# Kernel optimization log

Hardware: AMD Instinct MI355X
Metric: run time of the kernel (lower is better)

Reference implementation:

```python
import jax, jax.numpy as jnp
import numpy as np

ALPHA, BETA, GAMMA = 1.0, 1.0, 0.7
WIN = 11
C1 = 0.01 ** 2
C2 = 0.03 ** 2


def get_sobel_kernels(n1=1, n2=2, n3=2):
    a = np.asarray
    Sx = a([[[-n1, 0, n1], [-n2, 0, n2], [-n1, 0, n1]],
            [[-n2, 0, n2], [-n3 * n2, 0, n3 * n2], [-n2, 0, n2]],
            [[-n1, 0, n1], [-n2, 0, n2], [-n1, 0, n1]]])
    Sy = a([[[-n1, -n2, -n1], [0, 0, 0], [n1, n2, n1]],
            [[-n2, -n3 * n2, -n2], [0, 0, 0], [n2, n3 * n2, n2]],
            [[-n1, -n2, -n1], [0, 0, 0], [n1, n2, n1]]])
    Sz = a([[[-n1, -n2, -n1], [-n2, -n3 * n2, -n2], [-n1, -n2, -n1]],
            [[0, 0, 0], [0, 0, 0], [0, 0, 0]],
            [[n1, n2, n1], [n2, n3 * n2, n2], [n1, n2, n1]]])
    Sd11 = a([[[0, n1, n2], [-n1, 0, n1], [-n2, -n1, 0]],
              [[0, n2, n2 * n3], [-n2, 0, n2], [-n2 * n3, -n2, 0]],
              [[0, n1, n2], [-n1, 0, n1], [-n2, -n1, 0]]])
    Sd12 = a([[[-n2, -n1, 0], [-n1, 0, n1], [0, n1, n2]],
              [[-n2 * n3, -n2, 0], [-n2, 0, n2], [0, n2, n2 * n3]],
              [[-n2, -n1, 0], [-n1, 0, n1], [0, n1, n2]]])
    Sd21 = Sd11.T
    Sd22 = Sd12.T
    Sd31 = a([-S.T for S in Sd11.T])
    Sd32 = a([S.T for S in Sd12.T])
    return np.stack([Sx, Sy, Sz, Sd11, Sd12, Sd21, Sd22, Sd31, Sd32]).astype(np.float32)

# (9,1,3,3,3) fused sobel bank -- single grouped conv instead of 9 launches
SOBEL_W = jnp.asarray(get_sobel_kernels()[:, None])


def _gauss1d():
    g = jnp.exp(-(jnp.arange(WIN, dtype=jnp.float32) - WIN // 2) ** 2 / (2 * 1.5 ** 2))
    return g / g.sum()

G1D = _gauss1d()


def conv3d(x, w):
    return jax.lax.conv_general_dilated(
        x, w, window_strides=(1, 1, 1), padding='SAME',
        dimension_numbers=('NCDHW', 'OIDHW', 'NCDHW'))


def gauss_filter(x):
    # separable 11-tap gaussian along D, H, W (== full 11^3 window, zero-padded SAME)
    x = conv3d(x, G1D.reshape(1, 1, WIN, 1, 1))
    x = conv3d(x, G1D.reshape(1, 1, 1, WIN, 1))
    x = conv3d(x, G1D.reshape(1, 1, 1, 1, WIN))
    return x


def edge_map(img):
    # GradEdge3D.__call__ with a=1, C=1
    B, C, D, H, W = img.shape
    xp = jnp.pad(img, ((0, 0), (0, 0), (1, 1), (1, 1), (1, 1)), mode='reflect')
    g = conv3d(xp, SOBEL_W)                       # (B, 9, D+2, H+2, W+2)
    gm = jnp.sqrt(jnp.sum((g + 1e-6) ** 2 + 1e-6, axis=1))  # (B, D+2, H+2, W+2)
    gm = gm[:, 1:-1, 1:-1, 1:-1]
    norm = (gm - gm.min()) / (gm.max() - gm.min() + 1e-6)
    return norm.reshape(B, 1, D, H, W)


def ssim_value(pred, target):
    mu_p = gauss_filter(pred)
    mu_t = gauss_filter(target)
    mu_p2, mu_t2, mu_pt = mu_p ** 2, mu_t ** 2, mu_p * mu_t
    sig_p = gauss_filter(pred * pred) - mu_p2
    sig_t = gauss_filter(target * target) - mu_t2
    sig_pt = gauss_filter(pred * target) - mu_pt
    ssim_map = ((2 * mu_pt + C1) * (2 * sig_pt + C2)) / ((mu_p2 + mu_t2 + C1) * (sig_p + sig_t + C2))
    return 1.0 - ssim_map.mean()


def setup_inputs() -> dict:
    key = jax.random.key(0)
    k1, k2 = jax.random.split(key)
    shape = (2, 1, 128, 128, 128)
    return {
        'pred': jax.random.uniform(k1, shape, dtype=jnp.float32),
        'target': jax.random.uniform(k2, shape, dtype=jnp.float32),
    }


def reference(pred, target):
    loss_mse = jnp.mean((pred - target) ** 2)
    loss_ssim = ssim_value(pred, target)
    # GMELoss3D: lam_errors=[(1.0, L1Loss())], reduction='sum'
    loss_gme = 1e-6 + jnp.mean(jnp.abs(edge_map(pred) - edge_map(target)))
    total = ALPHA * loss_mse + BETA * loss_ssim + GAMMA * loss_gme
    return (total, loss_mse, loss_ssim, loss_gme)
```

## Files before the change

kernel.cpp:

```cpp
#include <hip/hip_runtime.h>


#define VOL 4194304
#define HV  2097152

typedef _Float16 h2 __attribute__((ext_vector_type(2)));
typedef _Float16 h4 __attribute__((ext_vector_type(4)));
typedef _Float16 h8 __attribute__((ext_vector_type(8)));

constexpr float GW[11] = {
    0.00102838f, 0.00759876f, 0.03600077f, 0.10936070f, 0.21300554f,
    0.26601173f,
    0.21300554f, 0.10936070f, 0.03600077f, 0.00759876f, 0.00102838f};



__device__ __forceinline__ void wblur_body(
    const float* __restrict__ p, const float* __restrict__ t,
    _Float16* __restrict__ A, double* __restrict__ mseB, const int bidx,
    char* __restrict__ pool, float* __restrict__ redw) {
  float (* __restrict__ sr)[138] = (float (*)[138])pool;
  float (* __restrict__ dr)[138] = (float (*)[138])(pool + 8832);
  const int tid = threadIdx.x;
  const int gbase = bidx << 11;
  if (tid < 160) {
    const int r = tid / 10, j = tid % 10;
    const int c = (j < 5) ? j : (128 + j);
    sr[r][c] = 0.f; dr[r][c] = 0.f;
  }
  float msel = 0.f;
#pragma unroll
  for (int i = 0; i < 8; ++i) {
    const int v = (i << 8) + tid;
    const float pv = p[gbase + v];
    const float tv = t[gbase + v];
    const float sv = pv + tv, dv = pv - tv;
    sr[v >> 7][5 + (v & 127)] = sv;
    dr[v >> 7][5 + (v & 127)] = dv;
    msel += dv * dv;
  }
  __syncthreads();
  h4* __restrict__ A4 = (h4*)A;
#pragma unroll
  for (int i = 0; i < 8; ++i) {
    const int v = (i << 8) + tid;
    const int row = v >> 7, x = v & 127;
    float as = 0.f, ad = 0.f, ass = 0.f, add_ = 0.f;
#pragma unroll
    for (int k = 0; k < 11; ++k) {
      const float w = GW[k];
      const float a = sr[row][x + k];
      const float b = dr[row][x + k];
      const float wa = w * a;
      const float wb = w * b;
      as += wa; ad += wb;
      ass += wa * a; add_ += wb * b;
    }
    h4 o;
    o[0] = (_Float16)as;  o[1] = (_Float16)ad;
    o[2] = (_Float16)ass; o[3] = (_Float16)add_;
    A4[gbase + v] = o;
  }
  redw[tid] = msel;
  __syncthreads();
  for (int s = 128; s > 0; s >>= 1) {
    if (tid < s) redw[tid] += redw[tid + s];
    __syncthreads();
  }
  if (tid == 0) atomicAdd(&mseB[(bidx & 63) << 3], (double)redw[0]);
}

__device__ __forceinline__ void sobel_body(
    const float* __restrict__ p, const float* __restrict__ t,
    _Float16* __restrict__ gmP, _Float16* __restrict__ gmT,
    unsigned int* __restrict__ ui, const int bx, const int by, const int bz,
    char* __restrict__ pool, float* __restrict__ rmin) {
  float* __restrict__ sb   = (float*)pool;
  float* __restrict__ rmax = (float*)(pool + 5184);
  const int tid = threadIdx.x;
  const int tx = tid & 15;
  const int ty = tid >> 4;
  const int x0 = bx << 4;
  const int y0 = by << 4;
  const int vol = bz >> 3;
  const int b   = (bz >> 2) & 1;
  const int z0  = (bz & 3) << 5;
  const float* __restrict__ img = vol ? t : p;
  _Float16* __restrict__ gm = vol ? gmT : gmP;
  const int vb = b << 21;

  const int ly1 = tid / 24, lx1 = tid % 24;
  const bool v1 = (lx1 < 18);
  int gy1 = y0 - 1 + ly1; gy1 = gy1 < 0 ? 1 : (gy1 > 127 ? 126 : gy1);
  int gx1 = x0 - 1 + lx1; gx1 = gx1 < 0 ? 1 : (gx1 > 127 ? 126 : gx1);
  const int off1 = (gy1 << 7) + gx1;
  const int s2i = tid + 256;
  const int ly2 = s2i / 24, lx2 = s2i % 24;
  const bool v2 = (s2i < 432) && (lx2 < 18);
  int gy2 = y0 - 1 + ly2; gy2 = gy2 < 0 ? 1 : (gy2 > 127 ? 126 : gy2);
  int gx2 = x0 - 1 + lx2; gx2 = gx2 < 0 ? 1 : (gx2 > 127 ? 126 : gx2);
  const int off2 = (gy2 << 7) + gx2;
  const int rb = ty * 24 + tx;
  const int gbase = vb + (z0 << 14) + ((y0 + ty) << 7) + (x0 + tx);

  float Y0[7], Y1[7], Y2[7];
  float rv1 = 0.f, rv2 = 0.f;
  float lmin = 3.4e38f, lmax = 0.f;

#define LOADR(ZS) {                                                         \
    const int zc_ = (ZS) > 127 ? 126 : (ZS);                                \
    const int za_ = vb + (zc_ << 14);                                       \
    if (v1) rv1 = img[za_ + off1];                                          \
    if (v2) rv2 = img[za_ + off2]; }

#define WRITELDS(BOFF) {                                                    \
    if (v1) sb[(BOFF) + tid] = rv1;                                         \
    if (v2) sb[(BOFF) + s2i] = rv2; }

#define COMPY(P) {                                                          \
    const int o_ = (P) * 432 + rb;                                          \
    const float r00 = sb[o_],      r01 = sb[o_ + 1],  r02 = sb[o_ + 2];     \
    const float r10 = sb[o_ + 24], r11 = sb[o_ + 25], r12 = sb[o_ + 26];    \
    const float r20 = sb[o_ + 48], r21 = sb[o_ + 49], r22 = sb[o_ + 50];    \
    const float dx0 = r02 - r00, dx1 = r12 - r10, dx2 = r22 - r20;          \
    const float ux0 = r00 + r01 + r02, ux1 = r10 + r11 + r12,               \
                ux2 = r20 + r21 + r22;                                      \
    const float sx0 = ux0 + r01, sx1 = ux1 + r11, sx2 = ux2 + r21;          \
    Y##P[1] = dx0 + dx1 + dx2;                                    \
    Y##P[0] = Y##P[1] + dx1;                                      \
    Y##P[2] = sx2 - sx0;                                          \
    Y##P[4] = sx0 + sx1 + sx2;                                    \
    Y##P[3] = Y##P[4] + sx1;                                      \
    Y##P[5] = ux2 - ux0;                                          \
    Y##P[6] = (ux0 + ux2) + 2.f * ux1; }

#define EMIT(I, P0, P1, P2) {                                               \
    const float E_ = Y##P0[0] + Y##P1[0] + Y##P2[0];                        \
    const float g1 = E_ + Y##P1[0];                                         \
    const float tA = Y##P0[1] + Y##P1[1] + Y##P2[1];                        \
    const float A_ = tA + Y##P1[1];                                         \
    const float D_ = Y##P0[2] + Y##P1[2] + Y##P2[2];                        \
    const float g2 = D_ + Y##P1[2];                                         \
    const float g3 = Y##P2[3] - Y##P0[3];                                   \
    const float C_ = Y##P2[4] - Y##P0[4];                                   \
    const float B_ = (Y##P0[5] + Y##P2[5]) + 2.f * Y##P1[5];                \
    const float F_ = Y##P2[6] - Y##P0[6];                                   \
    const float g4 = A_ - B_, g5 = A_ + B_;                                 \
    const float g6 = C_ - D_, g7 = C_ + D_;                                 \
    const float g8 = E_ - F_, g9 = E_ + F_;                                 \
    float ss_ = 9e-6f, t_;                                                  \
    t_ = g1 + 1e-6f; ss_ = fmaf(t_, t_, ss_);                               \
    t_ = g2 + 1e-6f; ss_ = fmaf(t_, t_, ss_);                               \
    t_ = g3 + 1e-6f; ss_ = fmaf(t_, t_, ss_);                               \
    t_ = g4 + 1e-6f; ss_ = fmaf(t_, t_, ss_);                               \
    t_ = g5 + 1e-6f; ss_ = fmaf(t_, t_, ss_);                               \
    t_ = g6 + 1e-6f; ss_ = fmaf(t_, t_, ss_);                               \
    t_ = g7 + 1e-6f; ss_ = fmaf(t_, t_, ss_);                               \
    t_ = g8 + 1e-6f; ss_ = fmaf(t_, t_, ss_);                               \
    t_ = g9 + 1e-6f; ss_ = fmaf(t_, t_, ss_);                               \
    const _Float16 gh = (_Float16)sqrtf(ss_);                               \
    gm[gbase + ((I) << 14)] = gh;                                           \
    const float gq = (float)gh;                                             \
    lmin = fminf(lmin, gq); lmax = fmaxf(lmax, gq); }

#define BODY(I, P0, P1, P2) {                                               \
    WRITELDS((P2) * 432);                                                   \
    LOADR(z0 + (I) + 2);                                                    \
    __syncthreads();                                                        \
    COMPY(P2);                                                              \
    EMIT(I, P0, P1, P2); }

  {
    const int zp = (z0 == 0) ? 1 : (z0 - 1);
    LOADR(zp);  WRITELDS(0);
    LOADR(z0);  WRITELDS(432);
    __syncthreads();
    COMPY(0);
    COMPY(1);
    LOADR(z0 + 1);
  }
  for (int ii = 0; ii < 30; ii += 3) {
    BODY(ii,     0, 1, 2);
    BODY(ii + 1, 1, 2, 0);
    BODY(ii + 2, 2, 0, 1);
  }
  BODY(30, 0, 1, 2);
  BODY(31, 1, 2, 0);

#undef BODY
#undef EMIT
#undef COMPY
#undef WRITELDS
#undef LOADR

  rmin[tid] = lmin; rmax[tid] = lmax;
  __syncthreads();
  for (int st = 128; st > 0; st >>= 1) {
    if (tid < st) {
      rmin[tid] = fminf(rmin[tid], rmin[tid + st]);
      rmax[tid] = fmaxf(rmax[tid], rmax[tid + st]);
    }
    __syncthreads();
  }
  if (tid == 0) {
    const int bin = (bx + (by << 3) + (bz << 6)) & 63;
    atomicMax(&ui[vol * 1024 + (bin << 4)], ~__float_as_uint(rmin[0]));
    atomicMax(&ui[2048 + vol * 1024 + (bin << 4)], __float_as_uint(rmax[0]));
  }
}

__device__ __forceinline__ void edge_body(
    const _Float16* __restrict__ gmP, const _Float16* __restrict__ gmT,
    const unsigned int* __restrict__ ui, double* __restrict__ absB,
    const int bidx, float* __restrict__ rede) {
  unsigned umnp = 0u, umnt = 0u, umxp = 0u, umxt = 0u;
  for (int j = 0; j < 64; ++j) {
    const unsigned a0 = ui[j << 4];
    const unsigned a1 = ui[1024 + (j << 4)];
    const unsigned a2 = ui[2048 + (j << 4)];
    const unsigned a3 = ui[3072 + (j << 4)];
    umnp = umnp > a0 ? umnp : a0;
    umnt = umnt > a1 ? umnt : a1;
    umxp = umxp > a2 ? umxp : a2;
    umxt = umxt > a3 ? umxt : a3;
  }
  const float mnp = __uint_as_float(~umnp);
  const float mnt = __uint_as_float(~umnt);
  const float mxp = __uint_as_float(umxp);
  const float mxt = __uint_as_float(umxt);
  const float scp = 1.f / (mxp - mnp + 1e-6f);
  const float sct = 1.f / (mxt - mnt + 1e-6f);
  const h8* __restrict__ gp = (const h8*)gmP;
  const h8* __restrict__ gt = (const h8*)gmT;
  float lsum = 0.f;
  const int base = bidx << 9;
#pragma unroll
  for (int i = 0; i < 2; ++i) {
    const int idx = base + (i << 8) + threadIdx.x;
    const h8 a = gp[idx];
    const h8 b = gt[idx];
#pragma unroll
    for (int j = 0; j < 8; ++j)
      lsum += fabsf(((float)a[j] - mnp) * scp - ((float)b[j] - mnt) * sct);
  }
  rede[threadIdx.x] = lsum;
  __syncthreads();
  for (int s = 128; s > 0; s >>= 1) {
    if (threadIdx.x < s) rede[threadIdx.x] += rede[threadIdx.x + s];
    __syncthreads();
  }
  if (threadIdx.x == 0)
    atomicAdd(&absB[(bidx & 63) << 3], (double)rede[0]);
}

__global__ __launch_bounds__(256) void k_fused_a(
    const float* __restrict__ p, const float* __restrict__ t,
    _Float16* __restrict__ A, double* __restrict__ mseB,
    _Float16* __restrict__ gmP, _Float16* __restrict__ gmT,
    unsigned int* __restrict__ ui) {
  __shared__ __align__(16) char pool[17664];
  __shared__ float redshared[256];
  const int bid = blockIdx.x;
  const int r3 = bid % 3;
  if (r3 < 2) {
    wblur_body(p, t, A, mseB, (bid / 3) * 2 + r3, pool, redshared);
  } else {
    const int s = bid / 3;
    sobel_body(p, t, gmP, gmT, ui, s & 7, (s >> 3) & 7, s >> 6,
               pool, redshared);
  }
}

__global__ __launch_bounds__(256) void k_fused_b(
    const _Float16* __restrict__ A, _Float16* __restrict__ B) {
  const int idx = blockIdx.x;
  const int z = idx & 127;
  const int yseg = (idx >> 7) & 7;
  const int batch = idx >> 10;
  const int tid = threadIdx.x;
  const int xc = tid & 63;
  const int yg = tid >> 6;
  const h8* __restrict__ Ah = (const h8*)A;
  h8* __restrict__ Bh = (h8*)B;
  const int slice8 = (batch << 20) + (z << 13);
  const int ybase = (yseg << 4) + (yg << 2);
  h8 acc0{}, acc1{}, acc2{}, acc3{};
#pragma unroll
  for (int k = 0; k < 14; ++k) {
    const int y = ybase - 5 + k;
    h8 rv{};
    if ((unsigned)y < 128u) rv = Ah[slice8 + (y << 6) + xc];
    if (k <= 10)           acc0 += (_Float16)GW[k]      * rv;
    if (k >= 1 && k <= 11) acc1 += (_Float16)GW[k - 1]  * rv;
    if (k >= 2 && k <= 12) acc2 += (_Float16)GW[k - 2]  * rv;
    if (k >= 3)            acc3 += (_Float16)GW[k - 3]  * rv;
  }
  const int wbase = slice8 + (ybase << 6) + xc;
  Bh[wbase]            = acc0;
  Bh[wbase + (1 << 6)] = acc1;
  Bh[wbase + (2 << 6)] = acc2;
  Bh[wbase + (3 << 6)] = acc3;
}

__global__ __launch_bounds__(256) void k_zblur_ssim(
    const _Float16* __restrict__ B, double* __restrict__ ssimB,
    const _Float16* __restrict__ gmP, const _Float16* __restrict__ gmT,
    const unsigned int* __restrict__ ui, double* __restrict__ absB) {
  __shared__ float red[256];
  const int tid = threadIdx.x;
  const int bid = blockIdx.x;
  const int r3 = bid % 3;
  if (r3 == 2) {
    edge_body(gmP, gmT, ui, absB, bid / 3, red);
    return;
  }
  const int idx = (bid / 3) * 2 + r3;
  const int y = idx & 127;
  const int zseg = (idx >> 7) & 7;
  const int batch = idx >> 10;
  const int xc = tid & 63;
  const int zg = tid >> 6;
  const h8* __restrict__ Bh = (const h8*)B;
  const int col8 = (batch << 20) + (y << 6);
  const int zbase = (zseg << 4) + (zg << 2);
  h8 m0{}, m1{}, m2{}, m3{};
#pragma unroll
  for (int k = 0; k < 14; ++k) {
    const int zz = zbase - 5 + k;
    h8 rv{};
    if ((unsigned)zz < 128u) rv = Bh[col8 + (zz << 13) + xc];
    if (k <= 10)           m0 += (_Float16)GW[k]      * rv;
    if (k >= 1 && k <= 11) m1 += (_Float16)GW[k - 1]  * rv;
    if (k >= 2 && k <= 12) m2 += (_Float16)GW[k - 2]  * rv;
    if (k >= 3)            m3 += (_Float16)GW[k - 3]  * rv;
  }
  float lsum = 0.f;
  h8 mv[4] = {m0, m1, m2, m3};
#pragma unroll
  for (int r = 0; r < 4; ++r) {
#pragma unroll
    for (int j = 0; j < 2; ++j) {
      const float mus = (float)mv[r][4 * j + 0];
      const float mud = (float)mv[r][4 * j + 1];
      const float ess = (float)mv[r][4 * j + 2];
      const float edd = (float)mv[r][4 * j + 3];
      const float S2 = mus * mus, D2 = mud * mud;
      const float num = ((S2 - D2) * 0.5f + 1e-4f) *
                        ((ess - edd - S2 + D2) * 0.5f + 9e-4f);
      const float den = ((S2 + D2) * 0.5f + 1e-4f) *
                        ((ess + edd - S2 - D2) * 0.5f + 9e-4f);
      lsum += num / den;
    }
  }
  red[tid] = lsum;
  __syncthreads();
  for (int st = 128; st > 0; st >>= 1) {
    if (tid < st) red[tid] += red[tid + st];
    __syncthreads();
  }
  if (tid == 0) {
    const int bin = idx & 63;
    atomicAdd(&ssimB[bin << 3], (double)red[0]);
  }
}

__global__ void k_final(const double* __restrict__ dbl, float* __restrict__ out) {
  if (threadIdx.x == 0 && blockIdx.x == 0) {
    double ms = 0.0, ss = 0.0, ab = 0.0;
    for (int j = 0; j < 64; ++j) {
      ms += dbl[j << 3];
      ss += dbl[512 + (j << 3)];
      ab += dbl[1024 + (j << 3)];
    }
    const double N = 4194304.0;
    const double mse   = ms / N;
    const double ssiml = 1.0 - ss / N;
    const double gme   = 1e-6 + ab / N;
    const double total = mse + ssiml + 0.7 * gme;
    out[0] = (float)total;
    out[1] = (float)mse;
    out[2] = (float)ssiml;
    out[3] = (float)gme;
  }
}

extern "C" void kernel_launch(void* const* d_in, const int* in_sizes, int n_in,
                              void* d_out, int out_size, void* d_ws, size_t ws_size,
                              hipStream_t stream) {
  const float* p = (const float*)d_in[0];
  const float* t = (const float*)d_in[1];
  _Float16* A = (_Float16*)d_ws;
  _Float16* B = A + (size_t)4 * VOL;
  char* accb = (char*)d_ws + (size_t)20 * VOL;
  double* dbl = (double*)accb;
  unsigned int* ui = (unsigned int*)(accb + 12288);
  _Float16* gmP = (_Float16*)((char*)d_ws + 88080384);
  _Float16* gmT = gmP + VOL;
  float* out = (float*)d_out;

  hipMemsetAsync(accb, 0, 28672, stream);
  k_fused_a<<<3072, 256, 0, stream>>>(p, t, A, dbl, gmP, gmT, ui);
  k_fused_b<<<2048, 256, 0, stream>>>(A, B);
  k_zblur_ssim<<<3072, 256, 0, stream>>>(B, dbl + 512, gmP, gmT, ui, dbl + 1024);
  k_final<<<1, 64, 0, stream>>>(dbl, out);
}
```

Baseline: 147.7 us.

## Merge stage kernels into one cooperative persistent kernel with grid syncs

Replaces the three stage kernels and the memset with one cooperative persistent kernel. Blocks loop over work units and meet at grid.sync barriers between the blur/sobel, y-blur/edge and z-blur/SSIM stages. Atomic accumulation into binned doubles and uint min/max is replaced by per-unit partial slots, which a block-reduced final kernel sums. This removes launch gaps and atomics, but adds grid-wide barrier cost, persistent-loop overhead, and each edge block now re-reduces 512 min/max partials.

```diff
diff --git a/kernel.cpp b/kernel.cpp
--- a/kernel.cpp
+++ b/kernel.cpp
@@ -1,4 +1,7 @@
 #include <hip/hip_runtime.h>
+#include <hip/hip_cooperative_groups.h>
+
+namespace cg = cooperative_groups;
 
 
 #define VOL 4194304
@@ -13,16 +16,14 @@
     0.26601173f,
     0.21300554f, 0.10936070f, 0.03600077f, 0.00759876f, 0.00102838f};
 
-
-
 __device__ __forceinline__ void wblur_body(
     const float* __restrict__ p, const float* __restrict__ t,
-    _Float16* __restrict__ A, double* __restrict__ mseB, const int bidx,
+    _Float16* __restrict__ A, double* __restrict__ mseS, const int unit,
     char* __restrict__ pool, float* __restrict__ redw) {
   float (* __restrict__ sr)[138] = (float (*)[138])pool;
   float (* __restrict__ dr)[138] = (float (*)[138])(pool + 8832);
   const int tid = threadIdx.x;
-  const int gbase = bidx << 11;
+  const int gbase = unit << 11;
   if (tid < 160) {
     const int r = tid / 10, j = tid % 10;
     const int c = (j < 5) ? j : (128 + j);
@@ -67,13 +68,14 @@
     if (tid < s) redw[tid] += redw[tid + s];
     __syncthreads();
   }
-  if (tid == 0) atomicAdd(&mseB[(bidx & 63) << 3], (double)redw[0]);
+  if (tid == 0) mseS[unit] = (double)redw[0];
 }
 
 __device__ __forceinline__ void sobel_body(
     const float* __restrict__ p, const float* __restrict__ t,
     _Float16* __restrict__ gmP, _Float16* __restrict__ gmT,
-    unsigned int* __restrict__ ui, const int bx, const int by, const int bz,
+    float* __restrict__ fminS, float* __restrict__ fmaxS,
+    const int bx, const int by, const int bz, const int sunit,
     char* __restrict__ pool, float* __restrict__ rmin) {
   float* __restrict__ sb   = (float*)pool;
   float* __restrict__ rmax = (float*)(pool + 5184);
@@ -203,77 +205,13 @@
     __syncthreads();
   }
   if (tid == 0) {
-    const int bin = (bx + (by << 3) + (bz << 6)) & 63;
-    atomicMax(&ui[vol * 1024 + (bin << 4)], ~__float_as_uint(rmin[0]));
-    atomicMax(&ui[2048 + vol * 1024 + (bin << 4)], __float_as_uint(rmax[0]));
-  }
-}
-
-__device__ __forceinline__ void edge_body(
-    const _Float16* __restrict__ gmP, const _Float16* __restrict__ gmT,
-    const unsigned int* __restrict__ ui, double* __restrict__ absB,
-    const int bidx, float* __restrict__ rede) {
-  unsigned umnp = 0u, umnt = 0u, umxp = 0u, umxt = 0u;
-  for (int j = 0; j < 64; ++j) {
-    const unsigned a0 = ui[j << 4];
-    const unsigned a1 = ui[1024 + (j << 4)];
-    const unsigned a2 = ui[2048 + (j << 4)];
-    const unsigned a3 = ui[3072 + (j << 4)];
-    umnp = umnp > a0 ? umnp : a0;
-    umnt = umnt > a1 ? umnt : a1;
-    umxp = umxp > a2 ? umxp : a2;
-    umxt = umxt > a3 ? umxt : a3;
-  }
-  const float mnp = __uint_as_float(~umnp);
-  const float mnt = __uint_as_float(~umnt);
-  const float mxp = __uint_as_float(umxp);
-  const float mxt = __uint_as_float(umxt);
-  const float scp = 1.f / (mxp - mnp + 1e-6f);
-  const float sct = 1.f / (mxt - mnt + 1e-6f);
-  const h8* __restrict__ gp = (const h8*)gmP;
-  const h8* __restrict__ gt = (const h8*)gmT;
-  float lsum = 0.f;
-  const int base = bidx << 9;
-#pragma unroll
-  for (int i = 0; i < 2; ++i) {
-    const int idx = base + (i << 8) + threadIdx.x;
-    const h8 a = gp[idx];
-    const h8 b = gt[idx];
-#pragma unroll
-    for (int j = 0; j < 8; ++j)
-      lsum += fabsf(((float)a[j] - mnp) * scp - ((float)b[j] - mnt) * sct);
-  }
-  rede[threadIdx.x] = lsum;
-  __syncthreads();
-  for (int s = 128; s > 0; s >>= 1) {
-    if (threadIdx.x < s) rede[threadIdx.x] += rede[threadIdx.x + s];
-    __syncthreads();
-  }
-  if (threadIdx.x == 0)
-    atomicAdd(&absB[(bidx & 63) << 3], (double)rede[0]);
-}
-
-__global__ __launch_bounds__(256) void k_fused_a(
-    const float* __restrict__ p, const float* __restrict__ t,
-    _Float16* __restrict__ A, double* __restrict__ mseB,
-    _Float16* __restrict__ gmP, _Float16* __restrict__ gmT,
-    unsigned int* __restrict__ ui) {
-  __shared__ __align__(16) char pool[17664];
-  __shared__ float redshared[256];
-  const int bid = blockIdx.x;
-  const int r3 = bid % 3;
-  if (r3 < 2) {
-    wblur_body(p, t, A, mseB, (bid / 3) * 2 + r3, pool, redshared);
-  } else {
-    const int s = bid / 3;
-    sobel_body(p, t, gmP, gmT, ui, s & 7, (s >> 3) & 7, s >> 6,
-               pool, redshared);
-  }
-}
-
-__global__ __launch_bounds__(256) void k_fused_b(
-    const _Float16* __restrict__ A, _Float16* __restrict__ B) {
-  const int idx = blockIdx.x;
+    fminS[sunit] = rmin[0];
+    fmaxS[sunit] = rmax[0];
+  }
+}
+
+__device__ __forceinline__ void blury_unit(
+    const _Float16* __restrict__ A, _Float16* __restrict__ B, const int idx) {
   const int z = idx & 127;
   const int yseg = (idx >> 7) & 7;
   const int batch = idx >> 10;
@@ -302,22 +240,66 @@
   Bh[wbase + (3 << 6)] = acc3;
 }
 
-__global__ __launch_bounds__(256) void k_zblur_ssim(
-    const _Float16* __restrict__ B, double* __restrict__ ssimB,
+__device__ __forceinline__ void edge_body(
     const _Float16* __restrict__ gmP, const _Float16* __restrict__ gmT,
-    const unsigned int* __restrict__ ui, double* __restrict__ absB) {
-  __shared__ float red[256];
-  const int tid = threadIdx.x;
-  const int bid = blockIdx.x;
-  const int r3 = bid % 3;
-  if (r3 == 2) {
-    edge_body(gmP, gmT, ui, absB, bid / 3, red);
-    return;
-  }
-  const int idx = (bid / 3) * 2 + r3;
-  const int y = idx & 127;
-  const int zseg = (idx >> 7) & 7;
-  const int batch = idx >> 10;
+    const float* __restrict__ fminS, const float* __restrict__ fmaxS,
+    double* __restrict__ absS, const int bidx,
+    char* __restrict__ pool, float* __restrict__ rede) {
+  float* __restrict__ rm0 = (float*)pool;
+  float* __restrict__ rM0 = rm0 + 256;
+  float* __restrict__ rm1 = rm0 + 512;
+  float* __restrict__ rM1 = rm0 + 768;
+  const int tid = threadIdx.x;
+  float mnp = 3.4e38f, mxp = 0.f, mnt = 3.4e38f, mxt = 0.f;
+  for (int j = tid; j < 512; j += 256) {
+    mnp = fminf(mnp, fminS[j]);
+    mxp = fmaxf(mxp, fmaxS[j]);
+    mnt = fminf(mnt, fminS[512 + j]);
+    mxt = fmaxf(mxt, fmaxS[512 + j]);
+  }
+  rm0[tid] = mnp; rM0[tid] = mxp; rm1[tid] = mnt; rM1[tid] = mxt;
+  __syncthreads();
+  for (int s = 128; s > 0; s >>= 1) {
+    if (tid < s) {
+      rm0[tid] = fminf(rm0[tid], rm0[tid + s]);
+      rM0[tid] = fmaxf(rM0[tid], rM0[tid + s]);
+      rm1[tid] = fminf(rm1[tid], rm1[tid + s]);
+      rM1[tid] = fmaxf(rM1[tid], rM1[tid + s]);
+    }
+    __syncthreads();
+  }
+  mnp = rm0[0]; mxp = rM0[0]; mnt = rm1[0]; mxt = rM1[0];
+  const float scp = 1.f / (mxp - mnp + 1e-6f);
+  const float sct = 1.f / (mxt - mnt + 1e-6f);
+  const h8* __restrict__ gp = (const h8*)gmP;
+  const h8* __restrict__ gt = (const h8*)gmT;
+  float lsum = 0.f;
+  const int base = bidx << 9;
+#pragma unroll
+  for (int i = 0; i < 2; ++i) {
+    const int idx = base + (i << 8) + tid;
+    const h8 a = gp[idx];
+    const h8 b = gt[idx];
+#pragma unroll
+    for (int j = 0; j < 8; ++j)
+      lsum += fabsf(((float)a[j] - mnp) * scp - ((float)b[j] - mnt) * sct);
+  }
+  rede[tid] = lsum;
+  __syncthreads();
+  for (int s = 128; s > 0; s >>= 1) {
+    if (tid < s) rede[tid] += rede[tid + s];
+    __syncthreads();
+  }
+  if (tid == 0) absS[bidx] = (double)rede[0];
+}
+
+__device__ __forceinline__ void zblur_unit(
+    const _Float16* __restrict__ B, double* __restrict__ ssimS, const int u,
+    float* __restrict__ red) {
+  const int y = u & 127;
+  const int zseg = (u >> 7) & 7;
+  const int batch = u >> 10;
+  const int tid = threadIdx.x;
   const int xc = tid & 63;
   const int zg = tid >> 6;
   const h8* __restrict__ Bh = (const h8*)B;
@@ -358,20 +340,68 @@
     if (tid < st) red[tid] += red[tid + st];
     __syncthreads();
   }
+  if (tid == 0) ssimS[u] = (double)red[0];
+}
+
+__global__ __launch_bounds__(256, 8) void k_pipeline(
+    const float* __restrict__ p, const float* __restrict__ t,
+    _Float16* __restrict__ A, _Float16* __restrict__ B,
+    double* __restrict__ mseS, double* __restrict__ ssimS,
+    double* __restrict__ absS, float* __restrict__ fminS,
+    float* __restrict__ fmaxS,
+    _Float16* __restrict__ gmP, _Float16* __restrict__ gmT) {
+  __shared__ __align__(16) char pool[17664];
+  __shared__ float red[256];
+  cg::grid_group grid = cg::this_grid();
+  const int nblk = gridDim.x;
+  for (int u = blockIdx.x; u < 3072; u += nblk) {
+    const int r3 = u % 3;
+    if (r3 < 2) {
+      wblur_body(p, t, A, mseS, (u / 3) * 2 + r3, pool, red);
+    } else {
+      const int s = u / 3;
+      sobel_body(p, t, gmP, gmT, fminS, fmaxS,
+                 s & 7, (s >> 3) & 7, s >> 6, s, pool, red);
+    }
+  }
+  grid.sync();
+  for (int u = blockIdx.x; u < 3072; u += nblk) {
+    const int r3 = u % 3;
+    if (r3 < 2) blury_unit(A, B, (u / 3) * 2 + r3);
+    else        edge_body(gmP, gmT, fminS, fmaxS, absS, u / 3, pool, red);
+  }
+  grid.sync();
+  for (int u = blockIdx.x; u < 2048; u += nblk)
+    zblur_unit(B, ssimS, u, red);
+}
+
+__global__ __launch_bounds__(256) void k_final(
+    const double* __restrict__ mseS, const double* __restrict__ ssimS,
+    const double* __restrict__ absS, float* __restrict__ out) {
+  __shared__ double dred[256];
+  const int tid = threadIdx.x;
+  double msl = 0.0, ssl = 0.0, abl = 0.0;
+  for (int j = tid; j < 2048; j += 256) { msl += mseS[j]; ssl += ssimS[j]; }
+  for (int j = tid; j < 1024; j += 256) abl += absS[j];
+  dred[tid] = msl; __syncthreads();
+  for (int s = 128; s > 0; s >>= 1) {
+    if (tid < s) dred[tid] += dred[tid + s];
+    __syncthreads();
+  }
+  const double ms = dred[0]; __syncthreads();
+  dred[tid] = ssl; __syncthreads();
+  for (int s = 128; s > 0; s >>= 1) {
+    if (tid < s) dred[tid] += dred[tid + s];
+    __syncthreads();
+  }
+  const double ss = dred[0]; __syncthreads();
+  dred[tid] = abl; __syncthreads();
+  for (int s = 128; s > 0; s >>= 1) {
+    if (tid < s) dred[tid] += dred[tid + s];
+    __syncthreads();
+  }
   if (tid == 0) {
-    const int bin = idx & 63;
-    atomicAdd(&ssimB[bin << 3], (double)red[0]);
-  }
-}
-
-__global__ void k_final(const double* __restrict__ dbl, float* __restrict__ out) {
-  if (threadIdx.x == 0 && blockIdx.x == 0) {
-    double ms = 0.0, ss = 0.0, ab = 0.0;
-    for (int j = 0; j < 64; ++j) {
-      ms += dbl[j << 3];
-      ss += dbl[512 + (j << 3)];
-      ab += dbl[1024 + (j << 3)];
-    }
+    const double ab = dred[0];
     const double N = 4194304.0;
     const double mse   = ms / N;
     const double ssiml = 1.0 - ss / N;
@@ -392,15 +422,30 @@
   _Float16* A = (_Float16*)d_ws;
   _Float16* B = A + (size_t)4 * VOL;
   char* accb = (char*)d_ws + (size_t)20 * VOL;
-  double* dbl = (double*)accb;
-  unsigned int* ui = (unsigned int*)(accb + 12288);
+  double* mseS  = (double*)accb;
+  double* ssimS = (double*)(accb + 16384);
+  double* absS  = (double*)(accb + 32768);
+  float*  fminS = (float*)(accb + 40960);
+  float*  fmaxS = (float*)(accb + 45056);
   _Float16* gmP = (_Float16*)((char*)d_ws + 88080384);
   _Float16* gmT = gmP + VOL;
   float* out = (float*)d_out;
 
-  hipMemsetAsync(accb, 0, 28672, stream);
-  k_fused_a<<<3072, 256, 0, stream>>>(p, t, A, dbl, gmP, gmT, ui);
-  k_fused_b<<<2048, 256, 0, stream>>>(A, B);
-  k_zblur_ssim<<<3072, 256, 0, stream>>>(B, dbl + 512, gmP, gmT, ui, dbl + 1024);
-  k_final<<<1, 64, 0, stream>>>(dbl, out);
-}
+  static int nblk = 0;
+  if (nblk == 0) {
+    int dev = 0, numCU = 0, maxBlk = 0;
+    hipGetDevice(&dev);
+    hipDeviceGetAttribute(&numCU, hipDeviceAttributeMultiprocessorCount, dev);
+    hipOccupancyMaxActiveBlocksPerMultiprocessor(&maxBlk, k_pipeline, 256, 0);
+    if (numCU <= 0) numCU = 256;
+    if (maxBlk <= 0) maxBlk = 1;
+    long cap = (long)maxBlk * (long)numCU;
+    nblk = (int)(cap < 2048 ? cap : 2048);
+  }
+  void* args[] = {(void*)&p, (void*)&t, (void*)&A, (void*)&B, (void*)&mseS,
+                  (void*)&ssimS, (void*)&absS, (void*)&fminS, (void*)&fmaxS,
+                  (void*)&gmP, (void*)&gmT};
+  hipLaunchCooperativeKernel(k_pipeline, dim3(nblk), dim3(256), args, 0,
+                             stream);
+  k_final<<<1, 256, 0, stream>>>(mseS, ssimS, absS, out);
+}
```

New measurement: 464.8 us. 215% more time.
